# Optimization experiments

Measured on AMD Instinct MI355X. Metric: run time of the kernel, lower is better.

Reference implementation:

```python
import jax, jax.numpy as jnp
import numpy as np

D = 256
H = 8
HD = D // H
LN_EPS = 1e-5


def setup_inputs() -> dict:
    key = jax.random.key(0)
    ks = jax.random.split(key, 20)
    N = 768
    s = lambda *sh: 1.0 / np.sqrt(sh[-1])
    inp = {
        "features": jax.random.normal(ks[0], (N, D), jnp.float32),
        "boxes": jax.random.uniform(ks[1], (N, 4), jnp.float32),
        # MultiheadAttention params (torch layout: [out, in])
        "in_proj_w": jax.random.normal(ks[2], (3 * D, D), jnp.float32) * s(D),
        "in_proj_b": jnp.zeros((3 * D,), jnp.float32),
        "out_proj_w": jax.random.normal(ks[3], (D, D), jnp.float32) * s(D),
        "out_proj_b": jnp.zeros((D,), jnp.float32),
        # similarity_net params
        "w1": jax.random.normal(ks[4], (256, 3 * D + 3), jnp.float32) * s(3 * D + 3),
        "b1": jnp.zeros((256,), jnp.float32),
        "ln_g": jnp.ones((256,), jnp.float32),
        "ln_b": jnp.zeros((256,), jnp.float32),
        "w2": jax.random.normal(ks[5], (128, 256), jnp.float32) * s(256),
        "b2": jnp.zeros((128,), jnp.float32),
        "w3": jax.random.normal(ks[6], (64, 128), jnp.float32) * s(128),
        "b3": jnp.zeros((64,), jnp.float32),
        "w4": jax.random.normal(ks[7], (32, 64), jnp.float32) * s(64),
        "b4": jnp.zeros((32,), jnp.float32),
        "w5": jax.random.normal(ks[8], (1, 32), jnp.float32) * s(32),
        "b5": jnp.zeros((1,), jnp.float32),
    }
    return inp


def _mha(x, in_w, in_b, out_w, out_b):
    # x: [N, D]; torch nn.MultiheadAttention self-attention (eval mode)
    N = x.shape[0]
    qkv = x @ in_w.T + in_b                      # [N, 3D]
    q, k, v = jnp.split(qkv, 3, axis=-1)
    q = q.reshape(N, H, HD).transpose(1, 0, 2)   # [H, N, HD]
    k = k.reshape(N, H, HD).transpose(1, 0, 2)
    v = v.reshape(N, H, HD).transpose(1, 0, 2)
    scores = jnp.einsum("hnd,hmd->hnm", q, k) / np.sqrt(HD)
    attn = jax.nn.softmax(scores, axis=-1)
    o = jnp.einsum("hnm,hmd->hnd", attn, v)      # [H, N, HD]
    o = o.transpose(1, 0, 2).reshape(N, D)
    return o @ out_w.T + out_b


def reference(features, boxes, in_proj_w, in_proj_b, out_proj_w, out_proj_b,
              w1, b1, ln_g, ln_b, w2, b2, w3, b3, w4, b4, w5, b5):
    N = features.shape[0]
    att = _mha(features, in_proj_w, in_proj_b, out_proj_w, out_proj_b)  # [N, D]

    fi = jnp.broadcast_to(att[:, None, :], (N, N, D))
    fj = jnp.broadcast_to(att[None, :, :], (N, N, D))
    bi = boxes[:, None, :]
    bj = boxes[None, :, :]
    x_dist = jnp.abs(bi[:, :, 0] - bj[:, :, 0])
    y_diff = bi[:, :, 1] - bj[:, :, 1]
    spatial = jnp.stack([x_dist, jnp.abs(y_diff), y_diff], axis=-1)    # [N, N, 3]
    pairs = jnp.concatenate([fi, fj, fi * fj, spatial], axis=-1)       # [N, N, 3D+3]

    h = jax.nn.relu(pairs @ w1.T + b1)
    mu = jnp.mean(h, axis=-1, keepdims=True)
    var = jnp.var(h, axis=-1, keepdims=True)
    h = (h - mu) / jnp.sqrt(var + LN_EPS) * ln_g + ln_b
    h = jax.nn.relu(h @ w2.T + b2)
    h = jax.nn.relu(h @ w3.T + b3)
    h = jax.nn.relu(h @ w4.T + b4)
    logits = (h @ w5.T + b5)[..., 0]                                   # [N, N]

    eye = jnp.eye(N, dtype=logits.dtype)
    return logits * (1.0 - eye) - 1e9 * eye
```

## Files before the change

### kernel.cpp

```cpp
#include <hip/hip_runtime.h>


typedef __attribute__((ext_vector_type(8))) __bf16 bf16x8;
typedef __attribute__((ext_vector_type(4))) float f32x4;

__device__ __forceinline__ float bf2f(unsigned short u) {
    return __uint_as_float(((unsigned int)u) << 16);
}
__device__ __forceinline__ unsigned short f2bf(float f) {
    union { __bf16 b; unsigned short u; } cv;
    cv.b = (__bf16)f;
    return cv.u;
}
__device__ __forceinline__ unsigned pk2(float lo, float hi) {
    return (unsigned)f2bf(lo) | ((unsigned)f2bf(hi) << 16);
}
__device__ __forceinline__ int pk4_fp8(float a, float b, float c, float d) {
    int w = __builtin_amdgcn_cvt_pk_fp8_f32(a, b, 0, false);
    w = __builtin_amdgcn_cvt_pk_fp8_f32(c, d, w, true);
    return w;
}
__device__ __forceinline__ unsigned char f2fp8(float v) {
    return (unsigned char)(__builtin_amdgcn_cvt_pk_fp8_f32(v, 0.f, 0, false) & 0xff);
}
__device__ __forceinline__ bf16x8 load8f_bf(const float* p) {
    float4 a = *reinterpret_cast<const float4*>(p);
    float4 b = *reinterpret_cast<const float4*>(p + 4);
    union { bf16x8 v; unsigned u[4]; } cv;
    cv.u[0] = pk2(a.x, a.y); cv.u[1] = pk2(a.z, a.w);
    cv.u[2] = pk2(b.x, b.y); cv.u[3] = pk2(b.z, b.w);
    return cv.v;
}

__global__ __launch_bounds__(256) void pack_all(
    const float* __restrict__ features, const float* __restrict__ in_proj_w,
    const float* __restrict__ in_proj_b, const float* __restrict__ out_proj_w,
    const float* __restrict__ w1, const float* __restrict__ w2,
    const float* __restrict__ w3, const float* __restrict__ w4,
    const float* __restrict__ b1, const float* __restrict__ ln_g,
    const float* __restrict__ ln_b, const float* __restrict__ b2,
    const float* __restrict__ out_proj_b,
    unsigned short* __restrict__ qkvb, unsigned short* __restrict__ Vt,
    unsigned short* __restrict__ WcatB,
    unsigned char* __restrict__ w1c_f8, unsigned char* __restrict__ w2g_f8,
    unsigned char* __restrict__ w3_f8, unsigned char* __restrict__ w4_f8,
    float* __restrict__ bias768, float* __restrict__ c1, float* __restrict__ c2)
{
    const int blk = blockIdx.x;
    if (blk < 716) {
        int t = blk * 256 + threadIdx.x;
        if (t < 65536) {
            WcatB[t] = f2bf(out_proj_w[t]);
        } else if (t < 139264) {
            int u = t - 65536;
            int e = u & 7, lane = (u >> 3) & 63, f = u >> 9;
            int l15 = lane & 15, quad = lane >> 4;
            int ct = f & 15, kc = f >> 4;
            int o = ct * 16 + l15, k = kc * 32 + quad * 8 + e;
            float v;
            if (k < 256)       v = w1[o * 771 + 512 + k];
            else if (k < 259)  v = w1[o * 771 + 768 + (k - 256)];
            else               v = 0.f;
            w1c_f8[u] = f2fp8(v);
        } else if (t < 172032) {
            int u = t - 139264;
            int e = u & 7, lane = (u >> 3) & 63, f = u >> 9;
            int l15 = lane & 15, quad = lane >> 4;
            int ct = f & 7, kc = f >> 3;
            int o = ct * 16 + l15, k = kc * 32 + quad * 8 + e;
            w2g_f8[u] = f2fp8(w2[o * 256 + k] * ln_g[k]);
        } else if (t < 180224) {
            int u = t - 172032;
            int e = u & 7, lane = (u >> 3) & 63, f = u >> 9;
            int l15 = lane & 15, quad = lane >> 4;
            int ct = f & 3, kc = f >> 2;
            int o = ct * 16 + l15, k = kc * 32 + quad * 8 + e;
            w3_f8[u] = f2fp8(w3[o * 128 + k]);
        } else if (t < 182272) {
            int u = t - 180224;
            int e = u & 7, lane = (u >> 3) & 63, f = u >> 9;
            int l15 = lane & 15, quad = lane >> 4;
            int ct = f & 1, kc = f >> 1;
            int o = ct * 16 + l15, k = kc * 32 + quad * 8 + e;
            w4_f8[u] = f2fp8(w4[o * 64 + k]);
        } else if (t < 183040) {
            int n = t - 182272;
            if (n < 256) bias768[n] = out_proj_b[n];
            else {
                int m = n - 256;
                float s = 0.f;
                for (int d = 0; d < 256; d += 4) {
                    float4 ob = *reinterpret_cast<const float4*>(&out_proj_b[d]);
                    const float* wr = (m < 256) ? &w1[m * 771 + d]
                                                : &w1[(m - 256) * 771 + 256 + d];
                    float4 w = *reinterpret_cast<const float4*>(wr);
                    s += ob.x * w.x + ob.y * w.y + ob.z * w.z + ob.w * w.w;
                }
                bias768[n] = s + ((m < 256) ? b1[m] : 0.f);
            }
        } else if (t < 183168) {
            int p = t - 183040;
            float s2 = 0.f, s1 = 0.f;
            for (int k = 0; k < 256; k += 4) {
                float4 w = *reinterpret_cast<const float4*>(&w2[p * 256 + k]);
                float4 g = *reinterpret_cast<const float4*>(&ln_g[k]);
                float4 lb = *reinterpret_cast<const float4*>(&ln_b[k]);
                s2 += g.x * w.x + g.y * w.y + g.z * w.z + g.w * w.w;
                s1 += lb.x * w.x + lb.y * w.y + lb.z * w.z + lb.w * w.w;
            }
            c2[p] = s2;
            c1[p] = s1 + b2[p];
        }
    } else if (blk < 1228) {
        const int n = blk - 716, e = threadIdx.x;
        const float* wrow = (n < 256) ? &w1[n * 771] : &w1[(n - 256) * 771 + 256];
        float acc = 0.f;
        for (int d = 0; d < 256; d += 4) {
            float4 w = *reinterpret_cast<const float4*>(&wrow[d]);
            acc += w.x * out_proj_w[(d + 0) * 256 + e];
            acc += w.y * out_proj_w[(d + 1) * 256 + e];
            acc += w.z * out_proj_w[(d + 2) * 256 + e];
            acc += w.w * out_proj_w[(d + 3) * 256 + e];
        }
        WcatB[(256 + n) * 256 + e] = f2bf(acc);
    } else {
        const int q = blk - 1228;
        const int bm = q % 12, bn = q / 12;
        const int wv = threadIdx.x >> 6, lane = threadIdx.x & 63;
        const int l15 = lane & 15, quad = lane >> 4;
        const int row0 = bm * 64 + wv * 16;
        const int col0 = bn * 64;
        f32x4 acc[4] = {};
        for (int kc = 0; kc < 8; ++kc) {
            bf16x8 a = load8f_bf(&features[(row0 + l15) * 256 + kc * 32 + quad * 8]);
#pragma unroll
            for (int ct = 0; ct < 4; ++ct) {
                bf16x8 b = load8f_bf(&in_proj_w[(col0 + ct * 16 + l15) * 256 + kc * 32 + quad * 8]);
                acc[ct] = __builtin_amdgcn_mfma_f32_16x16x32_bf16(a, b, acc[ct], 0, 0, 0);
            }
        }
#pragma unroll
        for (int ct = 0; ct < 4; ++ct)
#pragma unroll
            for (int r = 0; r < 4; ++r) {
                int row = row0 + quad * 4 + r, col = col0 + ct * 16 + l15;
                float v = acc[ct][r] + in_proj_b[col];
                if (col < 512) qkvb[row * 768 + col] = f2bf(v);
                else           Vt[(col - 512) * 768 + row] = f2bf(v);
            }
    }
}

__global__ __launch_bounds__(256) void gemm_attab(
    const unsigned short* __restrict__ A, const unsigned short* __restrict__ W,
    const float* __restrict__ bias, float* __restrict__ att,
    float* __restrict__ AB)
{
    const int wv = threadIdx.x >> 6, lane = threadIdx.x & 63;
    const int l15 = lane & 15, quad = lane >> 4;
    const int row0 = blockIdx.x * 64 + wv * 16;
    const int col0 = blockIdx.y * 64;
    f32x4 acc[4] = {};
    for (int kc = 0; kc < 8; ++kc) {
        bf16x8 a = *reinterpret_cast<const bf16x8*>(&A[(row0 + l15) * 256 + kc * 32 + quad * 8]);
#pragma unroll
        for (int ct = 0; ct < 4; ++ct) {
            bf16x8 b = *reinterpret_cast<const bf16x8*>(&W[(col0 + ct * 16 + l15) * 256 + kc * 32 + quad * 8]);
            acc[ct] = __builtin_amdgcn_mfma_f32_16x16x32_bf16(a, b, acc[ct], 0, 0, 0);
        }
    }
#pragma unroll
    for (int ct = 0; ct < 4; ++ct)
#pragma unroll
        for (int r = 0; r < 4; ++r) {
            int row = row0 + quad * 4 + r, col = col0 + ct * 16 + l15;
            float v = acc[ct][r] + bias[col];
            if (col < 256) att[row * 256 + col] = v;
            else           AB[row * 512 + (col - 256)] = v;
        }
}

#define SP 776

__global__ __launch_bounds__(256) void attn_mfma(
    const unsigned short* __restrict__ qkvb, const unsigned short* __restrict__ Vt,
    unsigned short* __restrict__ Obf)
{
    __shared__ __align__(16) unsigned short smS[32 * SP];
    const int h = blockIdx.x, q0 = blockIdx.y * 32, hb = h * 32;
    const int tid = threadIdx.x, wave = tid >> 6, lane = tid & 63;
    const int l15 = lane & 15, quad = lane >> 4;

    bf16x8 af[2];
#pragma unroll
    for (int mt = 0; mt < 2; ++mt)
        af[mt] = *reinterpret_cast<const bf16x8*>(&qkvb[(q0 + mt * 16 + l15) * 768 + hb + quad * 8]);
#pragma unroll
    for (int ct = 0; ct < 12; ++ct) {
        int n0 = wave * 192 + ct * 16;
        bf16x8 b = *reinterpret_cast<const bf16x8*>(&qkvb[(n0 + l15) * 768 + 256 + hb + quad * 8]);
#pragma unroll
        for (int mt = 0; mt < 2; ++mt) {
            f32x4 c = {};
            c = __builtin_amdgcn_mfma_f32_16x16x32_bf16(af[mt], b, c, 0, 0, 0);
#pragma unroll
            for (int r = 0; r < 4; ++r)
                smS[(mt * 16 + quad * 4 + r) * SP + n0 + l15] =
                    f2bf(c[r] * 0.17677669529663689f);
        }
    }
    __syncthreads();

    {
        const int row = tid >> 3, part = tid & 7;
        unsigned short* rp = &smS[row * SP + part * 96];
        float mx = -3.0e38f;
#pragma unroll
        for (int c8 = 0; c8 < 12; ++c8) {
            uint4 v = *reinterpret_cast<const uint4*>(&rp[c8 * 8]);
            const unsigned short* pe = reinterpret_cast<const unsigned short*>(&v);
#pragma unroll
            for (int e = 0; e < 8; ++e) mx = fmaxf(mx, bf2f(pe[e]));
        }
        mx = fmaxf(mx, __shfl_xor(mx, 1, 64));
        mx = fmaxf(mx, __shfl_xor(mx, 2, 64));
        mx = fmaxf(mx, __shfl_xor(mx, 4, 64));
        float ls = 0.f;
#pragma unroll
        for (int c8 = 0; c8 < 12; ++c8) {
            uint4 v = *reinterpret_cast<const uint4*>(&rp[c8 * 8]);
            const unsigned short* pe = reinterpret_cast<const unsigned short*>(&v);
            unsigned short o8[8];
#pragma unroll
            for (int e = 0; e < 8; ++e) {
                float ev = __expf(bf2f(pe[e]) - mx);
                ls += ev;
                o8[e] = f2bf(ev);
            }
            *reinterpret_cast<uint4*>(&rp[c8 * 8]) = *reinterpret_cast<const uint4*>(o8);
        }
        ls += __shfl_xor(ls, 1, 64);
        ls += __shfl_xor(ls, 2, 64);
        ls += __shfl_xor(ls, 4, 64);
        float inv = 1.0f / ls;
#pragma unroll
        for (int c8 = 0; c8 < 12; ++c8) {
            uint4 v = *reinterpret_cast<const uint4*>(&rp[c8 * 8]);
            const unsigned short* pe = reinterpret_cast<const unsigned short*>(&v);
            unsigned short o8[8];
#pragma unroll
            for (int e = 0; e < 8; ++e) o8[e] = f2bf(bf2f(pe[e]) * inv);
            *reinterpret_cast<uint4*>(&rp[c8 * 8]) = *reinterpret_cast<const uint4*>(o8);
        }
    }
    __syncthreads();

    const int row0 = (wave >> 1) * 16, cg = wave & 1;
    f32x4 accp = {};
    for (int kc = 0; kc < 24; ++kc) {
        bf16x8 a = *reinterpret_cast<const bf16x8*>(&smS[(row0 + l15) * SP + kc * 32 + quad * 8]);
        bf16x8 b = *reinterpret_cast<const bf16x8*>(&Vt[(hb + cg * 16 + l15) * 768 + kc * 32 + quad * 8]);
        accp = __builtin_amdgcn_mfma_f32_16x16x32_bf16(a, b, accp, 0, 0, 0);
    }
#pragma unroll
    for (int r = 0; r < 4; ++r) {
        int row = q0 + row0 + quad * 4 + r;
        Obf[row * 256 + hb + cg * 16 + l15] = f2bf(accp[r]);
    }
}

#define S1 296
#define S2 136
#define S3 72

__global__ __launch_bounds__(256, 4) void pair_mlp(
    const float* __restrict__ att, const float* __restrict__ AB,
    const unsigned char* __restrict__ w1c_f8, const unsigned char* __restrict__ w2g_f8,
    const unsigned char* __restrict__ w3_f8, const unsigned char* __restrict__ w4_f8,
    const float* __restrict__ boxes,
    const float* __restrict__ c1, const float* __restrict__ c2,
    const float* __restrict__ b3, const float* __restrict__ b4,
    const float* __restrict__ w5, const float* __restrict__ b5,
    float* __restrict__ out)
{
    __shared__ __align__(16) unsigned char smH[64 * S1];
    __shared__ __align__(16) unsigned char smH2[64 * S2];
    __shared__ __align__(16) unsigned char smH3[64 * S3];
    __shared__ float s_psum[64][4], s_pssq[64][4];
    __shared__ float s_mu[64], s_rs[64];
    __shared__ float s_l5[64][2];

    const int i    = blockIdx.x;
    const int j0   = blockIdx.y * 64;
    const int tid  = threadIdx.x;
    const int wave = tid >> 6;
    const int lane = tid & 63;
    const int l15  = lane & 15;
    const int quad = lane >> 4;

    {
        const int g = tid & 63;
        float4 fi4 = *reinterpret_cast<const float4*>(&att[i * 256 + g * 4]);
#pragma unroll
        for (int it = 0; it < 16; ++it) {
            int r = (tid >> 6) + it * 4;
            float4 aj = *reinterpret_cast<const float4*>(&att[(j0 + r) * 256 + g * 4]);
            *reinterpret_cast<int*>(&smH[r * S1 + g * 4]) =
                pk4_fp8(aj.x * fi4.x, aj.y * fi4.y, aj.z * fi4.z, aj.w * fi4.w);
        }
    }
    if (tid < 64) {
        int j = j0 + tid;
        float xd = fabsf(boxes[i * 4 + 0] - boxes[j * 4 + 0]);
        float yd = boxes[i * 4 + 1] - boxes[j * 4 + 1];
        *reinterpret_cast<int*>(&smH[tid * S1 + 256]) = pk4_fp8(xd, fabsf(yd), yd, 0.f);
        *reinterpret_cast<int*>(&smH[tid * S1 + 260]) = 0;
        *reinterpret_cast<long long*>(&smH[tid * S1 + 264]) = 0;
        *reinterpret_cast<long long*>(&smH[tid * S1 + 272]) = 0;
        *reinterpret_cast<long long*>(&smH[tid * S1 + 280]) = 0;
    }
    __syncthreads();

    f32x4 acc1[4][4] = {};
    for (int kc = 0; kc < 9; ++kc) {
        long long a[4];
#pragma unroll
        for (int mt = 0; mt < 4; ++mt)
            a[mt] = *reinterpret_cast<const long long*>(&w1c_f8[((kc * 16 + wave * 4 + mt) * 64 + lane) * 8]);
#pragma unroll
        for (int nt = 0; nt < 4; ++nt) {
            long long b = *reinterpret_cast<const long long*>(&smH[(nt * 16 + l15) * S1 + kc * 32 + quad * 8]);
#pragma unroll
            for (int mt = 0; mt < 4; ++mt)
                acc1[mt][nt] = __builtin_amdgcn_mfma_f32_16x16x32_fp8_fp8(a[mt], b, acc1[mt][nt], 0, 0, 0);
        }
    }

    const int o0 = wave * 64;
    float vsum[4] = {}, vssq[4] = {};
#pragma unroll
    for (int mt = 0; mt < 4; ++mt) {
        int o = o0 + mt * 16 + quad * 4;
        float4 Ai = *reinterpret_cast<const float4*>(&AB[i * 512 + o]);
        float AiA[4] = {Ai.x, Ai.y, Ai.z, Ai.w};
#pragma unroll
        for (int nt = 0; nt < 4; ++nt) {
            int j = nt * 16 + l15;
            float4 Bj = *reinterpret_cast<const float4*>(&AB[(j0 + j) * 512 + 256 + o]);
            float BjA[4] = {Bj.x, Bj.y, Bj.z, Bj.w};
#pragma unroll
            for (int r = 0; r < 4; ++r) {
                float v = fmaxf(acc1[mt][nt][r] + AiA[r] + BjA[r], 0.f);
                acc1[mt][nt][r] = v;
                vsum[nt] += v; vssq[nt] += v * v;
            }
        }
    }
#pragma unroll
    for (int nt = 0; nt < 4; ++nt) {
        vsum[nt] += __shfl_xor(vsum[nt], 16, 64);
        vsum[nt] += __shfl_xor(vsum[nt], 32, 64);
        vssq[nt] += __shfl_xor(vssq[nt], 16, 64);
        vssq[nt] += __shfl_xor(vssq[nt], 32, 64);
    }
    if (quad == 0)
#pragma unroll
        for (int nt = 0; nt < 4; ++nt) {
            s_psum[nt * 16 + l15][wave] = vsum[nt];
            s_pssq[nt * 16 + l15][wave] = vssq[nt];
        }
    __syncthreads();
#pragma unroll
    for (int mt = 0; mt < 4; ++mt) {
        int o = o0 + mt * 16 + quad * 4;
#pragma unroll
        for (int nt = 0; nt < 4; ++nt) {
            int j = nt * 16 + l15;
            *reinterpret_cast<int*>(&smH[j * S1 + o]) =
                pk4_fp8(acc1[mt][nt][0], acc1[mt][nt][1], acc1[mt][nt][2], acc1[mt][nt][3]);
        }
    }
    if (wave == 0) {
        int j = lane;
        float sm = (s_psum[j][0] + s_psum[j][1] + s_psum[j][2] + s_psum[j][3]) * (1.0f / 256.0f);
        float sq = (s_pssq[j][0] + s_pssq[j][1] + s_pssq[j][2] + s_pssq[j][3]) * (1.0f / 256.0f);
        s_mu[j] = sm;
        s_rs[j] = rsqrtf(sq - sm * sm + 1e-5f);
    }
    __syncthreads();

    f32x4 acc2[2][4] = {};
    for (int kc = 0; kc < 8; ++kc) {
        long long a[2];
#pragma unroll
        for (int mt = 0; mt < 2; ++mt)
            a[mt] = *reinterpret_cast<const long long*>(&w2g_f8[((kc * 8 + wave * 2 + mt) * 64 + lane) * 8]);
#pragma unroll
        for (int nt = 0; nt < 4; ++nt) {
            long long b = *reinterpret_cast<const long long*>(&smH[(nt * 16 + l15) * S1 + kc * 32 + quad * 8]);
#pragma unroll
            for (int mt = 0; mt < 2; ++mt)
                acc2[mt][nt] = __builtin_amdgcn_mfma_f32_16x16x32_fp8_fp8(a[mt], b, acc2[mt][nt], 0, 0, 0);
        }
    }
#pragma unroll
    for (int mt = 0; mt < 2; ++mt) {
        int p = wave * 32 + mt * 16 + quad * 4;
        float4 C1 = *reinterpret_cast<const float4*>(&c1[p]);
        float4 C2 = *reinterpret_cast<const float4*>(&c2[p]);
        float C1A[4] = {C1.x, C1.y, C1.z, C1.w};
        float C2A[4] = {C2.x, C2.y, C2.z, C2.w};
#pragma unroll
        for (int nt = 0; nt < 4; ++nt) {
            int j = nt * 16 + l15;
            float mu = s_mu[j], rs = s_rs[j];
            float vv[4];
#pragma unroll
            for (int r = 0; r < 4; ++r)
                vv[r] = fmaxf(rs * (acc2[mt][nt][r] - mu * C2A[r]) + C1A[r], 0.f);
            *reinterpret_cast<int*>(&smH2[j * S2 + p]) = pk4_fp8(vv[0], vv[1], vv[2], vv[3]);
        }
    }
    __syncthreads();

    f32x4 acc3[4] = {};
    for (int kc = 0; kc < 4; ++kc) {
        long long a = *reinterpret_cast<const long long*>(&w3_f8[((kc * 4 + wave) * 64 + lane) * 8]);
#pragma unroll
        for (int nt = 0; nt < 4; ++nt) {
            long long b = *reinterpret_cast<const long long*>(&smH2[(nt * 16 + l15) * S2 + kc * 32 + quad * 8]);
            acc3[nt] = __builtin_amdgcn_mfma_f32_16x16x32_fp8_fp8(a, b, acc3[nt], 0, 0, 0);
        }
    }
    {
        int q = wave * 16 + quad * 4;
        float4 B3 = *reinterpret_cast<const float4*>(&b3[q]);
        float B3A[4] = {B3.x, B3.y, B3.z, B3.w};
#pragma unroll
        for (int nt = 0; nt < 4; ++nt) {
            int j = nt * 16 + l15;
            float vv[4];
#pragma unroll
            for (int r = 0; r < 4; ++r)
                vv[r] = fmaxf(acc3[nt][r] + B3A[r], 0.f);
            *reinterpret_cast<int*>(&smH3[j * S3 + q]) = pk4_fp8(vv[0], vv[1], vv[2], vv[3]);
        }
    }
    __syncthreads();

    const int mt4 = wave & 1;
    const int jh  = wave >> 1;
    f32x4 acc4[2] = {};
#pragma unroll
    for (int kc = 0; kc < 2; ++kc) {
        long long a = *reinterpret_cast<const long long*>(&w4_f8[((kc * 2 + mt4) * 64 + lane) * 8]);
#pragma unroll
        for (int nt = 0; nt < 2; ++nt) {
            int j = jh * 32 + nt * 16 + l15;
            long long b = *reinterpret_cast<const long long*>(&smH3[j * S3 + kc * 32 + quad * 8]);
            acc4[nt] = __builtin_amdgcn_mfma_f32_16x16x32_fp8_fp8(a, b, acc4[nt], 0, 0, 0);
        }
    }
    {
        int o4 = mt4 * 16 + quad * 4;
        float4 B4 = *reinterpret_cast<const float4*>(&b4[o4]);
        float4 W5 = *reinterpret_cast<const float4*>(&w5[o4]);
        float B4A[4] = {B4.x, B4.y, B4.z, B4.w};
        float W5A[4] = {W5.x, W5.y, W5.z, W5.w};
#pragma unroll
        for (int nt = 0; nt < 2; ++nt) {
            float part = 0.f;
#pragma unroll
            for (int r = 0; r < 4; ++r)
                part += fmaxf(acc4[nt][r] + B4A[r], 0.f) * W5A[r];
            part += __shfl_xor(part, 16, 64);
            part += __shfl_xor(part, 32, 64);
            if (quad == 0)
                s_l5[jh * 32 + nt * 16 + l15][mt4] = part;
        }
    }
    __syncthreads();
    if (tid < 64) {
        int j = j0 + tid;
        float v = s_l5[tid][0] + s_l5[tid][1] + b5[0];
        out[i * 768 + j] = (j == i) ? -1.0e9f : v;
    }
}

extern "C" void kernel_launch(void* const* d_in, const int* in_sizes, int n_in,
                              void* d_out, int out_size, void* d_ws, size_t ws_size,
                              hipStream_t stream)
{
    const float* features   = (const float*)d_in[0];
    const float* boxes      = (const float*)d_in[1];
    const float* in_proj_w  = (const float*)d_in[2];
    const float* in_proj_b  = (const float*)d_in[3];
    const float* out_proj_w = (const float*)d_in[4];
    const float* out_proj_b = (const float*)d_in[5];
    const float* w1  = (const float*)d_in[6];
    const float* b1  = (const float*)d_in[7];
    const float* ln_g = (const float*)d_in[8];
    const float* ln_b = (const float*)d_in[9];
    const float* w2  = (const float*)d_in[10];
    const float* b2  = (const float*)d_in[11];
    const float* w3  = (const float*)d_in[12];
    const float* b3  = (const float*)d_in[13];
    const float* w4  = (const float*)d_in[14];
    const float* b4  = (const float*)d_in[15];
    const float* w5  = (const float*)d_in[16];
    const float* b5  = (const float*)d_in[17];
    float* out = (float*)d_out;

    char* p = (char*)d_ws;
    unsigned short* qkvb  = (unsigned short*)p; p += 768 * 768 * 2;
    unsigned short* Vt    = (unsigned short*)p; p += 256 * 768 * 2;
    unsigned short* Obf   = (unsigned short*)p; p += 768 * 256 * 2;
    unsigned short* WcatB = (unsigned short*)p; p += 196608 * 2;
    float* att = (float*)p; p += 768 * 256 * 4;
    float* AB  = (float*)p; p += 768 * 512 * 4;
    unsigned char* w1c_f8  = (unsigned char*)p; p += 73728;
    unsigned char* w2g_f8  = (unsigned char*)p; p += 32768;
    unsigned char* w3_f8   = (unsigned char*)p; p += 8192;
    unsigned char* w4_f8   = (unsigned char*)p; p += 2048;
    float* bias768 = (float*)p; p += 768 * 4;
    float* c1v     = (float*)p; p += 128 * 4;
    float* c2v     = (float*)p; p += 128 * 4;

    pack_all<<<dim3(1372), dim3(256), 0, stream>>>(features, in_proj_w,
        in_proj_b, out_proj_w, w1, w2, w3, w4, b1, ln_g, ln_b, b2, out_proj_b,
        qkvb, Vt, WcatB, w1c_f8, w2g_f8, w3_f8, w4_f8, bias768, c1v, c2v);
    attn_mfma<<<dim3(8, 24), dim3(256), 0, stream>>>(qkvb, Vt, Obf);
    gemm_attab<<<dim3(12, 12), dim3(256), 0, stream>>>(Obf, WcatB, bias768,
        att, AB);
    pair_mlp<<<dim3(768, 12), dim3(256), 0, stream>>>(att, AB,
        w1c_f8, w2g_f8, w3_f8, w4_f8, boxes, c1v, c2v,
        b3, b4, w5, b5, out);
}
```

Before: 301.2 us.

## Use MX-scaled 16x16x128 fp8 MFMA for pair MLP layers 1-3

Replaces the 16x16x32 fp8 MFMA loops in the first three pair-MLP layers with the gfx950 scaled 16x16x128 f8f6f4 MFMA, using unit scales. Weights are repacked in pack_all to match the 32-byte-per-lane operand layout, and the 3-wide spatial tail of layer 1 is split into a separate small 16x16x32 MFMA pass. LDS row strides are widened to keep the 16-byte reads aligned and avoid bank conflicts. The goal is fewer MFMA issues and fewer LDS/global loads per tile, at the cost of 32-byte register operands and more register pressure.

```diff
diff --git a/kernel.cpp b/kernel.cpp
--- a/kernel.cpp
+++ b/kernel.cpp
@@ -3,6 +3,7 @@
 
 typedef __attribute__((ext_vector_type(8))) __bf16 bf16x8;
 typedef __attribute__((ext_vector_type(4))) float f32x4;
+typedef __attribute__((ext_vector_type(8))) int i32x8;
 
 __device__ __forceinline__ float bf2f(unsigned short u) {
     return __uint_as_float(((unsigned int)u) << 16);
@@ -31,6 +32,15 @@
     cv.u[2] = pk2(b.x, b.y); cv.u[3] = pk2(b.z, b.w);
     return cv.v;
 }
+__device__ __forceinline__ i32x8 ld32_lds(const unsigned char* p) {
+    union { i32x8 v; uint4 q[2]; } r;
+    r.q[0] = *reinterpret_cast<const uint4*>(p);
+    r.q[1] = *reinterpret_cast<const uint4*>(p + 16);
+    return r.v;
+}
+#define SC1 0x7F7F7F7F
+#define MFMA_MX(a, b, c) __builtin_amdgcn_mfma_scale_f32_16x16x128_f8f6f4( \
+        (a), (b), (c), 0, 0, 0, SC1, 0, SC1)
 
 __global__ __launch_bounds__(256) void pack_all(
     const float* __restrict__ features, const float* __restrict__ in_proj_w,
@@ -42,8 +52,9 @@
     const float* __restrict__ out_proj_b,
     unsigned short* __restrict__ qkvb, unsigned short* __restrict__ Vt,
     unsigned short* __restrict__ WcatB,
-    unsigned char* __restrict__ w1c_f8, unsigned char* __restrict__ w2g_f8,
-    unsigned char* __restrict__ w3_f8, unsigned char* __restrict__ w4_f8,
+    unsigned char* __restrict__ w1c_mx, unsigned char* __restrict__ w1t_f8,
+    unsigned char* __restrict__ w2g_mx, unsigned char* __restrict__ w3_mx,
+    unsigned char* __restrict__ w4_f8,
     float* __restrict__ bias768, float* __restrict__ c1, float* __restrict__ c2)
 {
     const int blk = blockIdx.x;
@@ -51,31 +62,33 @@
         int t = blk * 256 + threadIdx.x;
         if (t < 65536) {
             WcatB[t] = f2bf(out_proj_w[t]);
+        } else if (t < 131072) {
+            int u = t - 65536;
+            int e = u & 31, lane = (u >> 5) & 63, f = u >> 11;
+            int mt = f & 15, ks = f >> 4;
+            int o = mt * 16 + (lane & 15);
+            int k = ks * 128 + ((lane >> 4) & 3) * 32 + e;
+            w1c_mx[u] = f2fp8(w1[o * 771 + 512 + k]);
         } else if (t < 139264) {
-            int u = t - 65536;
+            int u = t - 131072;
             int e = u & 7, lane = (u >> 3) & 63, f = u >> 9;
-            int l15 = lane & 15, quad = lane >> 4;
-            int ct = f & 15, kc = f >> 4;
-            int o = ct * 16 + l15, k = kc * 32 + quad * 8 + e;
-            float v;
-            if (k < 256)       v = w1[o * 771 + 512 + k];
-            else if (k < 259)  v = w1[o * 771 + 768 + (k - 256)];
-            else               v = 0.f;
-            w1c_f8[u] = f2fp8(v);
+            int o = f * 16 + (lane & 15);
+            int k = ((lane >> 4) & 3) * 8 + e;
+            float v = (k < 3) ? w1[o * 771 + 768 + k] : 0.f;
+            w1t_f8[u] = f2fp8(v);
         } else if (t < 172032) {
             int u = t - 139264;
-            int e = u & 7, lane = (u >> 3) & 63, f = u >> 9;
-            int l15 = lane & 15, quad = lane >> 4;
-            int ct = f & 7, kc = f >> 3;
-            int o = ct * 16 + l15, k = kc * 32 + quad * 8 + e;
-            w2g_f8[u] = f2fp8(w2[o * 256 + k] * ln_g[k]);
+            int e = u & 31, lane = (u >> 5) & 63, f = u >> 11;
+            int mt = f & 7, ks = f >> 3;
+            int p = mt * 16 + (lane & 15);
+            int k = ks * 128 + ((lane >> 4) & 3) * 32 + e;
+            w2g_mx[u] = f2fp8(w2[p * 256 + k] * ln_g[k]);
         } else if (t < 180224) {
             int u = t - 172032;
-            int e = u & 7, lane = (u >> 3) & 63, f = u >> 9;
-            int l15 = lane & 15, quad = lane >> 4;
-            int ct = f & 3, kc = f >> 2;
-            int o = ct * 16 + l15, k = kc * 32 + quad * 8 + e;
-            w3_f8[u] = f2fp8(w3[o * 128 + k]);
+            int e = u & 31, lane = (u >> 5) & 63, f = u >> 11;
+            int o = f * 16 + (lane & 15);
+            int k = ((lane >> 4) & 3) * 32 + e;
+            w3_mx[u] = f2fp8(w3[o * 128 + k]);
         } else if (t < 182272) {
             int u = t - 180224;
             int e = u & 7, lane = (u >> 3) & 63, f = u >> 9;
@@ -269,14 +282,15 @@
     }
 }
 
-#define S1 296
-#define S2 136
+#define S1 304
+#define S2 144
 #define S3 72
 
 __global__ __launch_bounds__(256, 4) void pair_mlp(
     const float* __restrict__ att, const float* __restrict__ AB,
-    const unsigned char* __restrict__ w1c_f8, const unsigned char* __restrict__ w2g_f8,
-    const unsigned char* __restrict__ w3_f8, const unsigned char* __restrict__ w4_f8,
+    const unsigned char* __restrict__ w1c_mx, const unsigned char* __restrict__ w1t_f8,
+    const unsigned char* __restrict__ w2g_mx, const unsigned char* __restrict__ w3_mx,
+    const unsigned char* __restrict__ w4_f8,
     const float* __restrict__ boxes,
     const float* __restrict__ c1, const float* __restrict__ c2,
     const float* __restrict__ b3, const float* __restrict__ b4,
@@ -322,14 +336,28 @@
     __syncthreads();
 
     f32x4 acc1[4][4] = {};
-    for (int kc = 0; kc < 9; ++kc) {
+#pragma unroll
+    for (int ks = 0; ks < 2; ++ks) {
+        i32x8 a[4];
+#pragma unroll
+        for (int mt = 0; mt < 4; ++mt)
+            a[mt] = *reinterpret_cast<const i32x8*>(&w1c_mx[((ks * 16 + wave * 4 + mt) * 64 + lane) * 32]);
+#pragma unroll
+        for (int nt = 0; nt < 4; ++nt) {
+            i32x8 b = ld32_lds(&smH[(nt * 16 + l15) * S1 + ks * 128 + quad * 32]);
+#pragma unroll
+            for (int mt = 0; mt < 4; ++mt)
+                acc1[mt][nt] = MFMA_MX(a[mt], b, acc1[mt][nt]);
+        }
+    }
+    {
         long long a[4];
 #pragma unroll
         for (int mt = 0; mt < 4; ++mt)
-            a[mt] = *reinterpret_cast<const long long*>(&w1c_f8[((kc * 16 + wave * 4 + mt) * 64 + lane) * 8]);
-#pragma unroll
-        for (int nt = 0; nt < 4; ++nt) {
-            long long b = *reinterpret_cast<const long long*>(&smH[(nt * 16 + l15) * S1 + kc * 32 + quad * 8]);
+            a[mt] = *reinterpret_cast<const long long*>(&w1t_f8[((wave * 4 + mt) * 64 + lane) * 8]);
+#pragma unroll
+        for (int nt = 0; nt < 4; ++nt) {
+            long long b = *reinterpret_cast<const long long*>(&smH[(nt * 16 + l15) * S1 + 256 + quad * 8]);
 #pragma unroll
             for (int mt = 0; mt < 4; ++mt)
                 acc1[mt][nt] = __builtin_amdgcn_mfma_f32_16x16x32_fp8_fp8(a[mt], b, acc1[mt][nt], 0, 0, 0);
@@ -390,17 +418,18 @@
     __syncthreads();
 
     f32x4 acc2[2][4] = {};
-    for (int kc = 0; kc < 8; ++kc) {
-        long long a[2];
+#pragma unroll
+    for (int ks = 0; ks < 2; ++ks) {
+        i32x8 a[2];
 #pragma unroll
         for (int mt = 0; mt < 2; ++mt)
-            a[mt] = *reinterpret_cast<const long long*>(&w2g_f8[((kc * 8 + wave * 2 + mt) * 64 + lane) * 8]);
-#pragma unroll
-        for (int nt = 0; nt < 4; ++nt) {
-            long long b = *reinterpret_cast<const long long*>(&smH[(nt * 16 + l15) * S1 + kc * 32 + quad * 8]);
+            a[mt] = *reinterpret_cast<const i32x8*>(&w2g_mx[((ks * 8 + wave * 2 + mt) * 64 + lane) * 32]);
+#pragma unroll
+        for (int nt = 0; nt < 4; ++nt) {
+            i32x8 b = ld32_lds(&smH[(nt * 16 + l15) * S1 + ks * 128 + quad * 32]);
 #pragma unroll
             for (int mt = 0; mt < 2; ++mt)
-                acc2[mt][nt] = __builtin_amdgcn_mfma_f32_16x16x32_fp8_fp8(a[mt], b, acc2[mt][nt], 0, 0, 0);
+                acc2[mt][nt] = MFMA_MX(a[mt], b, acc2[mt][nt]);
         }
     }
 #pragma unroll
@@ -424,12 +453,12 @@
     __syncthreads();
 
     f32x4 acc3[4] = {};
-    for (int kc = 0; kc < 4; ++kc) {
-        long long a = *reinterpret_cast<const long long*>(&w3_f8[((kc * 4 + wave) * 64 + lane) * 8]);
-#pragma unroll
-        for (int nt = 0; nt < 4; ++nt) {
-            long long b = *reinterpret_cast<const long long*>(&smH2[(nt * 16 + l15) * S2 + kc * 32 + quad * 8]);
-            acc3[nt] = __builtin_amdgcn_mfma_f32_16x16x32_fp8_fp8(a, b, acc3[nt], 0, 0, 0);
+    {
+        i32x8 a = *reinterpret_cast<const i32x8*>(&w3_mx[(wave * 64 + lane) * 32]);
+#pragma unroll
+        for (int nt = 0; nt < 4; ++nt) {
+            i32x8 b = ld32_lds(&smH2[(nt * 16 + l15) * S2 + quad * 32]);
+            acc3[nt] = MFMA_MX(a, b, acc3[nt]);
         }
     }
     {
@@ -518,21 +547,23 @@
     unsigned short* WcatB = (unsigned short*)p; p += 196608 * 2;
     float* att = (float*)p; p += 768 * 256 * 4;
     float* AB  = (float*)p; p += 768 * 512 * 4;
-    unsigned char* w1c_f8  = (unsigned char*)p; p += 73728;
-    unsigned char* w2g_f8  = (unsigned char*)p; p += 32768;
-    unsigned char* w3_f8   = (unsigned char*)p; p += 8192;
-    unsigned char* w4_f8   = (unsigned char*)p; p += 2048;
+    unsigned char* w1c_mx = (unsigned char*)p; p += 65536;
+    unsigned char* w1t_f8 = (unsigned char*)p; p += 8192;
+    unsigned char* w2g_mx = (unsigned char*)p; p += 32768;
+    unsigned char* w3_mx  = (unsigned char*)p; p += 8192;
+    unsigned char* w4_f8  = (unsigned char*)p; p += 2048;
     float* bias768 = (float*)p; p += 768 * 4;
     float* c1v     = (float*)p; p += 128 * 4;
     float* c2v     = (float*)p; p += 128 * 4;
 
     pack_all<<<dim3(1372), dim3(256), 0, stream>>>(features, in_proj_w,
         in_proj_b, out_proj_w, w1, w2, w3, w4, b1, ln_g, ln_b, b2, out_proj_b,
-        qkvb, Vt, WcatB, w1c_f8, w2g_f8, w3_f8, w4_f8, bias768, c1v, c2v);
+        qkvb, Vt, WcatB, w1c_mx, w1t_f8, w2g_mx, w3_mx, w4_f8,
+        bias768, c1v, c2v);
     attn_mfma<<<dim3(8, 24), dim3(256), 0, stream>>>(qkvb, Vt, Obf);
     gemm_attab<<<dim3(12, 12), dim3(256), 0, stream>>>(Obf, WcatB, bias768,
         att, AB);
     pair_mlp<<<dim3(768, 12), dim3(256), 0, stream>>>(att, AB,
-        w1c_f8, w2g_f8, w3_f8, w4_f8, boxes, c1v, c2v,
+        w1c_mx, w1t_f8, w2g_mx, w3_mx, w4_f8, boxes, c1v, c2v,
         b3, b4, w5, b5, out);
 }
```

Result: faster. 291.1 us (-3.3%).
